# Kernel tuning notes

Hardware: AMD Instinct MI355X
Metric: run time of the kernel (lower is better)

The kernel has to match this reference:

```python
import jax, jax.numpy as jnp
import numpy as np

B, N = 2, 256
RC = 6.0
BOX = 12.0
# (center_radius, eta) for G2; kappas for G3; (eta, zeta, lambda) for G4/G5
G2_PARAMS = [(rs, eta) for rs in (0.0, 2.0) for eta in (0.1, 1.0)]
G3_KAPPAS = [1.0, 2.0]
G45_PARAMS = [(eta, zeta, lam) for eta in (0.01, 0.1) for zeta in (1.0, 4.0) for lam in (-1.0, 1.0)]


def _fc(r, rc):
    # Behler cosine cutoff: 0.5*(cos(pi r / rc) + 1) for r < rc, else 0
    return 0.5 * (jnp.cos(jnp.pi * r / rc) + 1.0) * (r < rc)


def setup_inputs() -> dict:
    key = jax.random.key(0)
    k1, k2 = jax.random.split(key)
    atomic_numbers = jax.random.randint(k1, (N,), 1, 10).astype(jnp.float32)
    coordinates = jax.random.uniform(k2, (B, N, 3), dtype=jnp.float32) * BOX
    return {"atomic_numbers": atomic_numbers, "coordinates": coordinates}


def reference(atomic_numbers, coordinates):
    b, n, _ = coordinates.shape
    # r_ij vector = x_i - x_j, matching coords.unsqueeze(-2) - coords.unsqueeze(-3)
    dvec = coordinates[:, :, None, :] - coordinates[:, None, :, :]        # [B,N,N,3]
    sq = jnp.sum(dvec * dvec, axis=-1)                                    # [B,N,N]
    pair_mask = ~jnp.eye(n, dtype=bool)                                   # j != i
    sq_safe = jnp.where(pair_mask, sq, 1.0)
    r = jnp.where(pair_mask, jnp.sqrt(sq_safe), 0.0)                      # [B,N,N]
    fcr = _fc(r, RC) * pair_mask                                          # cutoff, self excluded

    feats = [jnp.broadcast_to(atomic_numbers, (b, n))]
    # G1: sum_j fc(r_ij)
    feats.append(jnp.sum(fcr, axis=-1))
    # G2: sum_j exp(-eta*(r_ij - Rs)^2) * fc(r_ij)
    for rs, eta in G2_PARAMS:
        feats.append(jnp.sum(jnp.exp(-eta * (r - rs) ** 2) * fcr, axis=-1))
    # G3: sum_j cos(kappa * r_ij) * fc(r_ij)
    for kappa in G3_KAPPAS:
        feats.append(jnp.sum(jnp.cos(kappa * r) * fcr, axis=-1))

    # shared angular (triplet) quantities, each [B,N,N,N]
    dot = jnp.einsum('bijc,bikc->bijk', dvec, dvec)
    denom = r[:, :, :, None] * r[:, :, None, :]
    cos_t = dot / jnp.where(denom > 0, denom, 1.0)
    sq_ij = sq[:, :, :, None]
    sq_ik = sq[:, :, None, :]
    sq_jk = sq[:, None, :, :]
    sq3 = sq_ij + sq_ik + sq_jk
    sq2 = sq_ij + sq_ik
    # fc products: fcr already zero on the diagonal, so fc3 vanishes whenever
    # j==i, k==i, or j==k (full triplet mask for G4)
    fc3 = fcr[:, :, :, None] * fcr[:, :, None, :] * fcr[:, None, :, :]
    fc2 = fcr[:, :, :, None] * fcr[:, :, None, :] * pair_mask[None, None, :, :]

    # G4: 2^(1-zeta) sum_{j!=k} (1+lam*cos)^zeta exp(-eta*(rij^2+rik^2+rjk^2)) fc fc fc
    for eta, zeta, lam in G45_PARAMS:
        ang = jnp.maximum(1.0 + lam * cos_t, 0.0) ** zeta
        feats.append((2.0 ** (1.0 - zeta)) * jnp.sum(ang * jnp.exp(-eta * sq3) * fc3, axis=(-2, -1)))
    # G5: 2^(1-zeta) sum_{j!=k} (1+lam*cos)^zeta exp(-eta*(rij^2+rik^2)) fc fc
    for eta, zeta, lam in G45_PARAMS:
        ang = jnp.maximum(1.0 + lam * cos_t, 0.0) ** zeta
        feats.append((2.0 ** (1.0 - zeta)) * jnp.sum(ang * jnp.exp(-eta * sq2) * fc2, axis=(-2, -1)))

    return jnp.stack(feats, axis=-1)  # [B, N, 24]
```

## Files before the change

kernel.cpp:

```cpp
#include <hip/hip_runtime.h>
#include <math.h>

#define NN 256
#define NF 24
#define RCUT 6.0f
#define PI_F 3.14159265358979323846f
#define NSEG 2

__global__ __launch_bounds__(256) void feat_kernel(
    const float* __restrict__ Z,
    const float* __restrict__ coords,
    float* __restrict__ out)
{
    const int i   = blockIdx.x;
    const int b   = blockIdx.y;
    const int seg = blockIdx.z;
    const int tid = threadIdx.x;
    const int lane = tid & 63;
    const int wave = tid >> 6;

    __shared__ float4 geo[NN];
    __shared__ float4 wgt[NN];
    __shared__ int wave_cnt[4];
    __shared__ float partials[4][23];

    const float* cb = coords + (size_t)b * NN * 3;
    const float xi = cb[i * 3 + 0], yi = cb[i * 3 + 1], zi = cb[i * 3 + 2];
    const float xj = cb[tid * 3 + 0], yj = cb[tid * 3 + 1], zj = cb[tid * 3 + 2];

    const float dx = xi - xj, dy = yi - yj, dz = zi - zj;
    const float r2 = dx * dx + dy * dy + dz * dz;
    const float r  = sqrtf(r2);
    const bool incut = (tid != i) && (r < RCUT);
    const float fc = incut ? 0.5f * (__cosf((PI_F / RCUT) * r) + 1.0f) : 0.0f;
    const float eA = __expf(-0.01f * r2);
    const float eB = __expf(-0.1f * r2);

    const unsigned long long bal = __ballot(incut);
    if (lane == 0) wave_cnt[wave] = __popcll(bal);
    __syncthreads();
    int base_slot = 0;
#pragma unroll
    for (int w = 0; w < 4; w++) if (w < wave) base_slot += wave_cnt[w];
    const int m = wave_cnt[0] + wave_cnt[1] + wave_cnt[2] + wave_cnt[3];
    if (incut) {
        const int p = base_slot + __popcll(bal & ((1ULL << lane) - 1ULL));
        geo[p] = make_float4(dx, dy, dz, 1.0f / r);
        wgt[p] = make_float4(fc, eA, eB, 0.0f);
    }

    float acc[23];
#pragma unroll
    for (int t = 0; t < 23; t++) acc[t] = 0.0f;

    if (seg == 0) {
        acc[0] = fc;
        acc[1] = __expf(-0.1f * r2) * fc;
        acc[2] = __expf(-1.0f * r2) * fc;
        const float d = r - 2.0f;
        acc[3] = __expf(-0.1f * d * d) * fc;
        acc[4] = __expf(-1.0f * d * d) * fc;
        acc[5] = __cosf(r) * fc;
        acc[6] = __cosf(2.0f * r) * fc;
    }

    __syncthreads();

    if (tid < m) {
        const float4 gj = geo[tid];
        const float4 wj = wgt[tid];

        const int Rfull = (m - 1) >> 1;
        const int h = (Rfull + 1) >> 1;
        const int t0 = (seg == 0) ? 1 : h + 1;
        const int t1 = (seg == 0) ? h : Rfull;

        for (int t = t0; t <= t1; ++t) {
            int kk = tid + t; if (kk >= m) kk -= m;
            const float4 g = geo[kk];
            const float4 w = wgt[kk];
            const float ddx = gj.x - g.x, ddy = gj.y - g.y, ddz = gj.z - g.z;
            const float sqjk = ddx * ddx + ddy * ddy + ddz * ddz;
            const float rjk = sqrtf(sqjk);
            const float fcjk = (rjk < RCUT) ? 0.5f * (__cosf((PI_F / RCUT) * rjk) + 1.0f) : 0.0f;
            const float dot = gj.x * g.x + gj.y * g.y + gj.z * g.z;
            const float cost = dot * gj.w * g.w;
            const float base = wj.x * w.x;
            const float f3 = base * fcjk;
            const float e2a = wj.y * w.y;
            const float e2b = wj.z * w.z;
            const float e3a = e2a * __expf(-0.01f * sqjk);
            const float e3b = e2b * __expf(-0.1f * sqjk);
            const float c1m = fmaxf(1.0f - cost, 0.0f);
            const float c1p = fmaxf(1.0f + cost, 0.0f);
            const float c2m = c1m * c1m, c2p = c1p * c1p;
            const float c4m = c2m * c2m, c4p = c2p * c2p;
            const float w3a = e3a * f3, w3b = e3b * f3;
            const float w2a = e2a * base, w2b = e2b * base;
            acc[7]  += c1m * w3a;  acc[8]  += c1p * w3a;
            acc[9]  += c4m * w3a;  acc[10] += c4p * w3a;
            acc[11] += c1m * w3b;  acc[12] += c1p * w3b;
            acc[13] += c4m * w3b;  acc[14] += c4p * w3b;
            acc[15] += c1m * w2a;  acc[16] += c1p * w2a;
            acc[17] += c4m * w2a;  acc[18] += c4p * w2a;
            acc[19] += c1m * w2b;  acc[20] += c1p * w2b;
            acc[21] += c4m * w2b;  acc[22] += c4p * w2b;
        }

        if (seg == 1 && (m & 1) == 0 && tid < (m >> 1)) {
            int kk = tid + (m >> 1);
            const float4 g = geo[kk];
            const float4 w = wgt[kk];
            const float ddx = gj.x - g.x, ddy = gj.y - g.y, ddz = gj.z - g.z;
            const float sqjk = ddx * ddx + ddy * ddy + ddz * ddz;
            const float rjk = sqrtf(sqjk);
            const float fcjk = (rjk < RCUT) ? 0.5f * (__cosf((PI_F / RCUT) * rjk) + 1.0f) : 0.0f;
            const float dot = gj.x * g.x + gj.y * g.y + gj.z * g.z;
            const float cost = dot * gj.w * g.w;
            const float base = wj.x * w.x;
            const float f3 = base * fcjk;
            const float e2a = wj.y * w.y;
            const float e2b = wj.z * w.z;
            const float e3a = e2a * __expf(-0.01f * sqjk);
            const float e3b = e2b * __expf(-0.1f * sqjk);
            const float c1m = fmaxf(1.0f - cost, 0.0f);
            const float c1p = fmaxf(1.0f + cost, 0.0f);
            const float c2m = c1m * c1m, c2p = c1p * c1p;
            const float c4m = c2m * c2m, c4p = c2p * c2p;
            const float w3a = e3a * f3, w3b = e3b * f3;
            const float w2a = e2a * base, w2b = e2b * base;
            acc[7]  += c1m * w3a;  acc[8]  += c1p * w3a;
            acc[9]  += c4m * w3a;  acc[10] += c4p * w3a;
            acc[11] += c1m * w3b;  acc[12] += c1p * w3b;
            acc[13] += c4m * w3b;  acc[14] += c4p * w3b;
            acc[15] += c1m * w2a;  acc[16] += c1p * w2a;
            acc[17] += c4m * w2a;  acc[18] += c4p * w2a;
            acc[19] += c1m * w2b;  acc[20] += c1p * w2b;
            acc[21] += c4m * w2b;  acc[22] += c4p * w2b;
        }
    }

#pragma unroll
    for (int t = 0; t < 23; t++) {
        float v = acc[t];
        for (int off = 32; off > 0; off >>= 1)
            v += __shfl_down(v, off, 64);
        if (lane == 0) partials[wave][t] = v;
    }
    __syncthreads();

    const size_t obase = ((size_t)b * NN + i) * NF;
    if (tid < 23) {
        float v = partials[0][tid] + partials[1][tid] + partials[2][tid] + partials[3][tid];
        if (tid >= 7) {
            const int a = (tid - 7) & 3;
            v *= (a >= 2) ? 0.25f : 2.0f;
        }
        atomicAdd(&out[obase + 1 + tid], v);
    } else if (tid == 23 && seg == 0) {
        out[obase] = Z[i];
    }
}

extern "C" void kernel_launch(void* const* d_in, const int* in_sizes, int n_in,
                              void* d_out, int out_size, void* d_ws, size_t ws_size,
                              hipStream_t stream) {
    const float* Z = (const float*)d_in[0];
    const float* coords = (const float*)d_in[1];
    float* out = (float*)d_out;
    hipMemsetAsync(out, 0, (size_t)out_size * sizeof(float), stream);
    dim3 grid(NN, 2, NSEG);
    dim3 block(NN);
    feat_kernel<<<grid, block, 0, stream>>>(Z, coords, out);
}
```

Measured before the change: 71.24 us.

## Use single-wave blocks with eight segments and a workspace reduction kernel

```diff
diff --git a/kernel.cpp b/kernel.cpp
--- a/kernel.cpp
+++ b/kernel.cpp
@@ -3,163 +3,143 @@
 
 #define NN 256
 #define NF 24
+#define NFEAT 23
 #define RCUT 6.0f
 #define PI_F 3.14159265358979323846f
-#define NSEG 2
+#define NSEG 8
 
-__global__ __launch_bounds__(256) void feat_kernel(
-    const float* __restrict__ Z,
+__device__ __forceinline__ void pair_body(const float4 gj, const float4 wj,
+                                          const float4 g, const float4 w,
+                                          float* acc)
+{
+    const float ddx = gj.x - g.x, ddy = gj.y - g.y, ddz = gj.z - g.z;
+    const float sqjk = ddx * ddx + ddy * ddy + ddz * ddz;
+    const float rjk = sqrtf(sqjk);
+    const float fcjk = (rjk < RCUT) ? 0.5f * (__cosf((PI_F / RCUT) * rjk) + 1.0f) : 0.0f;
+    const float dot = gj.x * g.x + gj.y * g.y + gj.z * g.z;
+    const float cost = dot * gj.w * g.w;
+    const float base = wj.x * w.x;
+    const float f3 = base * fcjk;
+    const float e2a = wj.y * w.y;
+    const float e2b = wj.z * w.z;
+    const float e3a = e2a * __expf(-0.01f * sqjk);
+    const float e3b = e2b * __expf(-0.1f * sqjk);
+    const float c1m = fmaxf(1.0f - cost, 0.0f);
+    const float c1p = fmaxf(1.0f + cost, 0.0f);
+    const float c2m = c1m * c1m, c2p = c1p * c1p;
+    const float c4m = c2m * c2m, c4p = c2p * c2p;
+    const float w3a = e3a * f3, w3b = e3b * f3;
+    const float w2a = e2a * base, w2b = e2b * base;
+    acc[7]  += c1m * w3a;  acc[8]  += c1p * w3a;
+    acc[9]  += c4m * w3a;  acc[10] += c4p * w3a;
+    acc[11] += c1m * w3b;  acc[12] += c1p * w3b;
+    acc[13] += c4m * w3b;  acc[14] += c4p * w3b;
+    acc[15] += c1m * w2a;  acc[16] += c1p * w2a;
+    acc[17] += c4m * w2a;  acc[18] += c4p * w2a;
+    acc[19] += c1m * w2b;  acc[20] += c1p * w2b;
+    acc[21] += c4m * w2b;  acc[22] += c4p * w2b;
+}
+
+__global__ __launch_bounds__(64) void feat_kernel(
     const float* __restrict__ coords,
-    float* __restrict__ out)
+    float* __restrict__ ws)
 {
-    const int i   = blockIdx.x;
-    const int b   = blockIdx.y;
-    const int seg = blockIdx.z;
-    const int tid = threadIdx.x;
-    const int lane = tid & 63;
-    const int wave = tid >> 6;
+    const int i    = blockIdx.x;
+    const int b    = blockIdx.y;
+    const int seg  = blockIdx.z;
+    const int lane = threadIdx.x;
 
     __shared__ float4 geo[NN];
     __shared__ float4 wgt[NN];
-    __shared__ int wave_cnt[4];
-    __shared__ float partials[4][23];
+    __shared__ float red[NFEAT];
 
     const float* cb = coords + (size_t)b * NN * 3;
     const float xi = cb[i * 3 + 0], yi = cb[i * 3 + 1], zi = cb[i * 3 + 2];
-    const float xj = cb[tid * 3 + 0], yj = cb[tid * 3 + 1], zj = cb[tid * 3 + 2];
 
-    const float dx = xi - xj, dy = yi - yj, dz = zi - zj;
-    const float r2 = dx * dx + dy * dy + dz * dz;
-    const float r  = sqrtf(r2);
-    const bool incut = (tid != i) && (r < RCUT);
-    const float fc = incut ? 0.5f * (__cosf((PI_F / RCUT) * r) + 1.0f) : 0.0f;
-    const float eA = __expf(-0.01f * r2);
-    const float eB = __expf(-0.1f * r2);
+    float acc[NFEAT];
+#pragma unroll
+    for (int t = 0; t < NFEAT; t++) acc[t] = 0.0f;
 
-    const unsigned long long bal = __ballot(incut);
-    if (lane == 0) wave_cnt[wave] = __popcll(bal);
-    __syncthreads();
-    int base_slot = 0;
+    int m = 0;
 #pragma unroll
-    for (int w = 0; w < 4; w++) if (w < wave) base_slot += wave_cnt[w];
-    const int m = wave_cnt[0] + wave_cnt[1] + wave_cnt[2] + wave_cnt[3];
-    if (incut) {
-        const int p = base_slot + __popcll(bal & ((1ULL << lane) - 1ULL));
-        geo[p] = make_float4(dx, dy, dz, 1.0f / r);
-        wgt[p] = make_float4(fc, eA, eB, 0.0f);
+    for (int rnd = 0; rnd < 4; ++rnd) {
+        const int j = lane + (rnd << 6);
+        const float xj = cb[j * 3 + 0], yj = cb[j * 3 + 1], zj = cb[j * 3 + 2];
+        const float dx = xi - xj, dy = yi - yj, dz = zi - zj;
+        const float r2 = dx * dx + dy * dy + dz * dz;
+        const float r  = sqrtf(r2);
+        const bool incut = (j != i) && (r < RCUT);
+        const float fc = incut ? 0.5f * (__cosf((PI_F / RCUT) * r) + 1.0f) : 0.0f;
+        if (seg == 0) {
+            acc[0] += fc;
+            acc[1] += __expf(-0.1f * r2) * fc;
+            acc[2] += __expf(-1.0f * r2) * fc;
+            const float d = r - 2.0f;
+            acc[3] += __expf(-0.1f * d * d) * fc;
+            acc[4] += __expf(-1.0f * d * d) * fc;
+            acc[5] += __cosf(r) * fc;
+            acc[6] += __cosf(2.0f * r) * fc;
+        }
+        const unsigned long long bal = __ballot(incut);
+        if (incut) {
+            const int p = m + __popcll(bal & ((1ULL << lane) - 1ULL));
+            geo[p] = make_float4(dx, dy, dz, 1.0f / r);
+            wgt[p] = make_float4(fc, __expf(-0.01f * r2), __expf(-0.1f * r2), 0.0f);
+        }
+        m += __popcll(bal);
     }
-
-    float acc[23];
-#pragma unroll
-    for (int t = 0; t < 23; t++) acc[t] = 0.0f;
-
-    if (seg == 0) {
-        acc[0] = fc;
-        acc[1] = __expf(-0.1f * r2) * fc;
-        acc[2] = __expf(-1.0f * r2) * fc;
-        const float d = r - 2.0f;
-        acc[3] = __expf(-0.1f * d * d) * fc;
-        acc[4] = __expf(-1.0f * d * d) * fc;
-        acc[5] = __cosf(r) * fc;
-        acc[6] = __cosf(2.0f * r) * fc;
-    }
-
     __syncthreads();
 
-    if (tid < m) {
-        const float4 gj = geo[tid];
-        const float4 wj = wgt[tid];
-
+    if (m >= 2) {
         const int Rfull = (m - 1) >> 1;
-        const int h = (Rfull + 1) >> 1;
-        const int t0 = (seg == 0) ? 1 : h + 1;
-        const int t1 = (seg == 0) ? h : Rfull;
-
-        for (int t = t0; t <= t1; ++t) {
-            int kk = tid + t; if (kk >= m) kk -= m;
-            const float4 g = geo[kk];
-            const float4 w = wgt[kk];
-            const float ddx = gj.x - g.x, ddy = gj.y - g.y, ddz = gj.z - g.z;
-            const float sqjk = ddx * ddx + ddy * ddy + ddz * ddz;
-            const float rjk = sqrtf(sqjk);
-            const float fcjk = (rjk < RCUT) ? 0.5f * (__cosf((PI_F / RCUT) * rjk) + 1.0f) : 0.0f;
-            const float dot = gj.x * g.x + gj.y * g.y + gj.z * g.z;
-            const float cost = dot * gj.w * g.w;
-            const float base = wj.x * w.x;
-            const float f3 = base * fcjk;
-            const float e2a = wj.y * w.y;
-            const float e2b = wj.z * w.z;
-            const float e3a = e2a * __expf(-0.01f * sqjk);
-            const float e3b = e2b * __expf(-0.1f * sqjk);
-            const float c1m = fmaxf(1.0f - cost, 0.0f);
-            const float c1p = fmaxf(1.0f + cost, 0.0f);
-            const float c2m = c1m * c1m, c2p = c1p * c1p;
-            const float c4m = c2m * c2m, c4p = c2p * c2p;
-            const float w3a = e3a * f3, w3b = e3b * f3;
-            const float w2a = e2a * base, w2b = e2b * base;
-            acc[7]  += c1m * w3a;  acc[8]  += c1p * w3a;
-            acc[9]  += c4m * w3a;  acc[10] += c4p * w3a;
-            acc[11] += c1m * w3b;  acc[12] += c1p * w3b;
-            acc[13] += c4m * w3b;  acc[14] += c4p * w3b;
-            acc[15] += c1m * w2a;  acc[16] += c1p * w2a;
-            acc[17] += c4m * w2a;  acc[18] += c4p * w2a;
-            acc[19] += c1m * w2b;  acc[20] += c1p * w2b;
-            acc[21] += c4m * w2b;  acc[22] += c4p * w2b;
-        }
-
-        if (seg == 1 && (m & 1) == 0 && tid < (m >> 1)) {
-            int kk = tid + (m >> 1);
-            const float4 g = geo[kk];
-            const float4 w = wgt[kk];
-            const float ddx = gj.x - g.x, ddy = gj.y - g.y, ddz = gj.z - g.z;
-            const float sqjk = ddx * ddx + ddy * ddy + ddz * ddz;
-            const float rjk = sqrtf(sqjk);
-            const float fcjk = (rjk < RCUT) ? 0.5f * (__cosf((PI_F / RCUT) * rjk) + 1.0f) : 0.0f;
-            const float dot = gj.x * g.x + gj.y * g.y + gj.z * g.z;
-            const float cost = dot * gj.w * g.w;
-            const float base = wj.x * w.x;
-            const float f3 = base * fcjk;
-            const float e2a = wj.y * w.y;
-            const float e2b = wj.z * w.z;
-            const float e3a = e2a * __expf(-0.01f * sqjk);
-            const float e3b = e2b * __expf(-0.1f * sqjk);
-            const float c1m = fmaxf(1.0f - cost, 0.0f);
-            const float c1p = fmaxf(1.0f + cost, 0.0f);
-            const float c2m = c1m * c1m, c2p = c1p * c1p;
-            const float c4m = c2m * c2m, c4p = c2p * c2p;
-            const float w3a = e3a * f3, w3b = e3b * f3;
-            const float w2a = e2a * base, w2b = e2b * base;
-            acc[7]  += c1m * w3a;  acc[8]  += c1p * w3a;
-            acc[9]  += c4m * w3a;  acc[10] += c4p * w3a;
-            acc[11] += c1m * w3b;  acc[12] += c1p * w3b;
-            acc[13] += c4m * w3b;  acc[14] += c4p * w3b;
-            acc[15] += c1m * w2a;  acc[16] += c1p * w2a;
-            acc[17] += c4m * w2a;  acc[18] += c4p * w2a;
-            acc[19] += c1m * w2b;  acc[20] += c1p * w2b;
-            acc[21] += c4m * w2b;  acc[22] += c4p * w2b;
+        const int tlo = 1 + (Rfull * seg) / NSEG;
+        const int thi = (Rfull * (seg + 1)) / NSEG;
+        const bool halfseg = (seg == NSEG - 1) && ((m & 1) == 0);
+        const int mh = m >> 1;
+        for (int rnd = 0; rnd < 4; ++rnd) {
+            const int jj = lane + (rnd << 6);
+            if (jj >= m) break;
+            const float4 gj = geo[jj];
+            const float4 wj = wgt[jj];
+            for (int t = tlo; t <= thi; ++t) {
+                int kk = jj + t; if (kk >= m) kk -= m;
+                pair_body(gj, wj, geo[kk], wgt[kk], acc);
+            }
+            if (halfseg && jj < mh)
+                pair_body(gj, wj, geo[jj + mh], wgt[jj + mh], acc);
         }
     }
 
 #pragma unroll
-    for (int t = 0; t < 23; t++) {
+    for (int t = 0; t < NFEAT; t++) {
         float v = acc[t];
         for (int off = 32; off > 0; off >>= 1)
             v += __shfl_down(v, off, 64);
-        if (lane == 0) partials[wave][t] = v;
+        if (lane == 0) red[t] = v;
     }
     __syncthreads();
+    if (lane < NFEAT)
+        ws[(((size_t)b * NN + i) * NSEG + seg) * NFEAT + lane] = red[lane];
+}
 
-    const size_t obase = ((size_t)b * NN + i) * NF;
-    if (tid < 23) {
-        float v = partials[0][tid] + partials[1][tid] + partials[2][tid] + partials[3][tid];
-        if (tid >= 7) {
-            const int a = (tid - 7) & 3;
-            v *= (a >= 2) ? 0.25f : 2.0f;
-        }
-        atomicAdd(&out[obase + 1 + tid], v);
-    } else if (tid == 23 && seg == 0) {
-        out[obase] = Z[i];
+__global__ __launch_bounds__(256) void reduce_kernel(
+    const float* __restrict__ Z,
+    const float* __restrict__ ws,
+    float* __restrict__ out)
+{
+    const int idx = blockIdx.x * 256 + threadIdx.x;
+    const int f  = idx % NF;
+    const int ai = idx / NF;
+    if (f == 0) { out[idx] = Z[ai & (NN - 1)]; return; }
+    float v = 0.0f;
+    const float* p = ws + ((size_t)ai * NSEG) * NFEAT + (f - 1);
+#pragma unroll
+    for (int s = 0; s < NSEG; ++s) v += p[s * NFEAT];
+    if (f >= 8) {
+        const int a = (f - 8) & 3;
+        v *= (a >= 2) ? 0.25f : 2.0f;
     }
+    out[idx] = v;
 }
 
 extern "C" void kernel_launch(void* const* d_in, const int* in_sizes, int n_in,
@@ -168,8 +148,9 @@
     const float* Z = (const float*)d_in[0];
     const float* coords = (const float*)d_in[1];
     float* out = (float*)d_out;
-    hipMemsetAsync(out, 0, (size_t)out_size * sizeof(float), stream);
+    float* ws = (float*)d_ws;
     dim3 grid(NN, 2, NSEG);
-    dim3 block(NN);
-    feat_kernel<<<grid, block, 0, stream>>>(Z, coords, out);
+    feat_kernel<<<grid, dim3(64), 0, stream>>>(coords, ws);
+    const int total = 2 * NN * NF;
+    reduce_kernel<<<total / 256, 256, 0, stream>>>(Z, ws, out);
 }
```

Result: slower. 72.92 us (+2.4%).
